# Performance work log

Hardware: AMD Instinct MI355X
Metric: run time of the kernel (lower is better)

Reference implementation:

```python
import jax, jax.numpy as jnp
import numpy as np

B, S, D, H = 2, 2048, 1024, 16
DK = D // H


def setup_inputs() -> dict:
    key = jax.random.key(0)
    ks = jax.random.split(key, 12)
    s = 1.0 / np.sqrt(D)
    return {
        "query": jax.random.normal(ks[0], (B, S, D), dtype=jnp.float32),
        "key": jax.random.normal(ks[1], (B, S, D), dtype=jnp.float32),
        "value": jax.random.normal(ks[2], (B, S, D), dtype=jnp.float32),
        "mask": jax.random.randint(ks[3], (B, 1, 1, S), 0, 2, dtype=jnp.int32),
        "wq": jax.random.normal(ks[4], (D, D), dtype=jnp.float32) * s,
        "bq": jnp.zeros((D,), dtype=jnp.float32),
        "wk": jax.random.normal(ks[5], (D, D), dtype=jnp.float32) * s,
        "bk": jnp.zeros((D,), dtype=jnp.float32),
        "wv": jax.random.normal(ks[6], (D, D), dtype=jnp.float32) * s,
        "bv": jnp.zeros((D,), dtype=jnp.float32),
        "wo": jax.random.normal(ks[7], (D, D), dtype=jnp.float32) * s,
        "bo": jnp.zeros((D,), dtype=jnp.float32),
    }


def reference(query, key, value, mask, wq, bq, wk, bk, wv, bv, wo, bo):
    b, s, d = query.shape
    # torch Linear: y = x @ W^T + b, then split heads -> [B, H, S, dk]
    def proj(x, w, bias):
        return (x @ w.T + bias).reshape(b, -1, H, DK).transpose(0, 2, 1, 3)

    q = proj(query, wq, bq)
    k = proj(key, wk, bk)
    v = proj(value, wv, bv)

    scores = jnp.einsum("bhqd,bhkd->bhqk", q, k) / jnp.sqrt(jnp.float32(DK))
    scores = jnp.where(mask == 0, jnp.float32(-1e9), scores)
    attn = jax.nn.softmax(scores, axis=-1)  # [B,H,S,S]
    x = jnp.einsum("bhqk,bhkd->bhqd", attn, v)
    x = x.transpose(0, 2, 1, 3).reshape(b, s, d)
    return x @ wo.T + bo
```

## Files before the change

kernel.cpp:

```cpp
#include <hip/hip_runtime.h>
#include <math.h>

#define B_  2
#define S_  2048
#define D_  1024
#define H_  16
#define DK_ 64

typedef unsigned short u16;
typedef unsigned int u32;
typedef __bf16 bf16x8 __attribute__((ext_vector_type(8)));
typedef float f32x4 __attribute__((ext_vector_type(4)));

typedef const __attribute__((address_space(1))) void* gas1_t;
typedef __attribute__((address_space(3))) void* las3_t;

__device__ __forceinline__ void gload_lds16(const void* g, void* l) {
    __builtin_amdgcn_global_load_lds((gas1_t)g, (las3_t)l, 16, 0, 0);
}

__device__ __forceinline__ u16 f2bf(float f) {
    union { float f; unsigned u; } v; v.f = f;
    return (u16)((v.u + 0x7fffu + ((v.u >> 16) & 1u)) >> 16);
}

__device__ __forceinline__ u32 pack_bf16_2(float lo, float hi) {
    union { float f; u32 u; } a, b;
    a.f = lo; b.f = hi;
    return __builtin_amdgcn_perm(b.u + 0x8000u, a.u + 0x8000u, 0x07060302u);
}

__global__ __launch_bounds__(256)
void cast_all(const float* __restrict__ q, const float* __restrict__ k,
              const float* __restrict__ v, const float* __restrict__ wq,
              const float* __restrict__ wk, const float* __restrict__ wv,
              const float* __restrict__ wo, const int* __restrict__ mask,
              u16* __restrict__ qb, u16* __restrict__ kb, u16* __restrict__ vb,
              u16* __restrict__ wqb, u16* __restrict__ wkb, u16* __restrict__ wvb,
              u16* __restrict__ wob, float* __restrict__ mfac,
              float* __restrict__ nmaskf)
{
    const int bi = blockIdx.x;
    const int tid = threadIdx.x;
    if (bi >= 16400) {
        const int b = bi - 16400;
        __shared__ int red[256];
        int c = 0;
#pragma unroll
        for (int j = 0; j < 8; ++j)
            c += (mask[b * S_ + tid * 8 + j] == 0) ? 1 : 0;
        red[tid] = c;
        __syncthreads();
        for (int s = 128; s > 0; s >>= 1) {
            if (tid < s) red[tid] += red[tid + s];
            __syncthreads();
        }
        if (tid == 0) nmaskf[b] = (float)red[0];
        return;
    }
    if (bi >= 16384) {
        const int idx = (bi - 16384) * 256 + tid;
        mfac[idx] = mask[idx] ? 1.0f : 0.0f;
        return;
    }
    const int i = bi * 256 + tid;
    const float* src; u16* dst; int off;
    if (i < 3 * 1048576) {
        const int seg = i >> 20; off = i & 1048575;
        src = (seg == 0) ? q : (seg == 1) ? k : v;
        dst = (seg == 0) ? qb : (seg == 1) ? kb : vb;
    } else {
        const int j = i - 3 * 1048576;
        const int seg = j >> 18; off = j & 262143;
        src = (seg == 0) ? wq : (seg == 1) ? wk : (seg == 2) ? wv : wo;
        dst = (seg == 0) ? wqb : (seg == 1) ? wkb : (seg == 2) ? wvb : wob;
    }
    const float4 val = ((const float4*)src)[off];
    uint2 o;
    o.x = pack_bf16_2(val.x, val.y);
    o.y = pack_bf16_2(val.z, val.w);
    ((uint2*)dst)[off] = o;
}

template<int BN>
__device__ __forceinline__ void gemm_body(
    const u16* __restrict__ A, const u16* __restrict__ W,
    const float* __restrict__ bias, void* __restrict__ outp,
    float scale, int mode, int m0, int n0,
    const float* __restrict__ rowfac, const float* __restrict__ colfac)
{
    constexpr int NJ = BN / 32;
    __shared__ u16 sA[128 * 64];
    __shared__ u16 sW[BN * 64];

    const int tid  = threadIdx.x;
    const int wave = tid >> 6, lane = tid & 63;
    const int quad = lane >> 4, l16 = lane & 15;
    const int wm = (wave >> 1) * 64;
    const int wn = (wave & 1) * (BN / 2);
    const int srow = lane >> 3;
    const int scol = ((lane & 7) ^ srow) * 8;
    const int sw7  = l16 & 7;

    f32x4 acc[4][NJ];
    const f32x4 zero = {0.f, 0.f, 0.f, 0.f};
#pragma unroll
    for (int i = 0; i < 4; ++i)
#pragma unroll
        for (int j = 0; j < NJ; ++j) acc[i][j] = zero;

    const u16* ast = A + (size_t)(m0 + wave * 8 + srow) * D_ + scol;
    const u16* wst = W + (size_t)(n0 + wave * 8 + srow) * D_ + scol;

    for (int k0 = 0; k0 < D_; k0 += 64) {
#pragma unroll
        for (int t = 0; t < 4; ++t)
            gload_lds16(ast + (size_t)t * 32 * D_ + k0, sA + (wave + t * 4) * 512);
        if (BN == 128) {
#pragma unroll
            for (int t = 0; t < 4; ++t)
                gload_lds16(wst + (size_t)t * 32 * D_ + k0, sW + (wave + t * 4) * 512);
        } else {
#pragma unroll
            for (int t = 0; t < 2; ++t)
                gload_lds16(wst + (size_t)t * 32 * D_ + k0, sW + (wave + t * 4) * 512);
        }
        __syncthreads();

#pragma unroll
        for (int kh = 0; kh < 2; ++kh) {
            const int phys = ((kh * 4 + quad) ^ sw7) * 8;
            bf16x8 af[4], bfr[NJ];
#pragma unroll
            for (int i = 0; i < 4; ++i)
                af[i] = *(const bf16x8*)(sA + (wm + i * 16 + l16) * 64 + phys);
#pragma unroll
            for (int j = 0; j < NJ; ++j)
                bfr[j] = *(const bf16x8*)(sW + (wn + j * 16 + l16) * 64 + phys);
#pragma unroll
            for (int i = 0; i < 4; ++i)
#pragma unroll
                for (int j = 0; j < NJ; ++j)
                    acc[i][j] = __builtin_amdgcn_mfma_f32_16x16x32_bf16(af[i], bfr[j], acc[i][j], 0, 0, 0);
        }
        __syncthreads();
    }

#pragma unroll
    for (int i = 0; i < 4; ++i) {
        float rf4[4];
        if (mode == 1 && rowfac) {
#pragma unroll
            for (int r = 0; r < 4; ++r)
                rf4[r] = rowfac[m0 + wm + i * 16 + quad * 4 + r];
        }
#pragma unroll
        for (int j = 0; j < NJ; ++j) {
            const int n = n0 + wn + j * 16 + l16;
            if (mode == 3) {
                const float cf = colfac ? colfac[n] : 1.0f;
#pragma unroll
                for (int r = 0; r < 4; ++r) {
                    const int mp = m0 + wm + i * 16 + quad * 4 + r;
                    ((u16*)outp)[(size_t)mp * (B_ * S_) + n] = f2bf((acc[i][j][r] + bias[mp]) * cf);
                }
            } else {
                const float bn = bias[n];
#pragma unroll
                for (int r = 0; r < 4; ++r) {
                    const int m = m0 + wm + i * 16 + quad * 4 + r;
                    float v = acc[i][j][r] + bn;
                    if (mode == 0) {
                        ((float*)outp)[(size_t)m * D_ + n] = v;
                    } else {
                        v *= scale;
                        if (rowfac) v *= rf4[r];
                        const int b = m >> 11, s = m & (S_ - 1);
                        const int h = n >> 6, dk = n & 63;
                        ((u16*)outp)[(((size_t)(b * H_ + h)) * S_ + s) * DK_ + dk] = f2bf(v);
                    }
                }
            }
        }
    }
}

__global__ __launch_bounds__(256)
void qkv_gemm(const u16* __restrict__ qin, const u16* __restrict__ kin, const u16* __restrict__ vin,
              const u16* __restrict__ wqb, const u16* __restrict__ wkb, const u16* __restrict__ wvb,
              const float* __restrict__ bq, const float* __restrict__ bk, const float* __restrict__ bv,
              u16* __restrict__ Qp, u16* __restrict__ Kp, u16* __restrict__ Vt,
              const float* __restrict__ mfac)
{
    const int z = blockIdx.z;
    if (z == 2) {
        gemm_body<128>(wvb, vin, bv, Vt, 1.0f, 3, blockIdx.x * 128, blockIdx.y * 128,
                       nullptr, mfac);
    } else {
        const u16* A = (z == 0) ? qin : kin;
        const u16* W = (z == 0) ? wqb : wkb;
        const float* bias = (z == 0) ? bq : bk;
        u16* outp = (z == 0) ? Qp : Kp;
        const float scale = (z == 0) ? 0.18033688011112042f : 1.0f;
        const float* rf = (z == 1) ? mfac : nullptr;
        gemm_body<128>(A, W, bias, outp, scale, 1, blockIdx.y * 128, blockIdx.x * 128,
                       rf, nullptr);
    }
}

__global__ __launch_bounds__(256)
void out_gemm(const u16* __restrict__ Xc, const u16* __restrict__ wob,
              const float* __restrict__ bo, float* __restrict__ out)
{
    gemm_body<64>(Xc, wob, bo, out, 1.0f, 0, blockIdx.y * 128, blockIdx.x * 64,
                  nullptr, nullptr);
}

__global__ __launch_bounds__(512, 4)
void attn_mfma(const u16* __restrict__ Qp, const u16* __restrict__ Kp,
               const u16* __restrict__ Vt, const float* __restrict__ nmaskf,
               u16* __restrict__ Xc)
{
    __shared__ u16 sPQ[8192];
    __shared__ u16 sKVraw[16384];

    const int tid  = threadIdx.x;
    const int wave = tid >> 6, lane = tid & 63;
    const int qg = wave & 3, kg = wave >> 2;
    const int quad = lane >> 4, l16 = lane & 15;
    const int qt = blockIdx.x & 15;
    const int bh = blockIdx.x >> 4;
    const int b  = bh >> 4;
    const int h  = bh & 15;
    const int lr  = lane >> 3;
    const int cl  = (lane & 7) ^ lr;
    const int sw7 = l16 & 7;

    const u16* Qb = Qp + ((size_t)bh * S_ + qt * 128) * DK_;
    const u16* Kb = Kp + (size_t)bh * S_ * DK_;
    const int vdk = (qg * 8 + lr) + 32 * (cl >> 2);
    const u16* Vsrc = Vt + (size_t)(h * 64 + vdk) * (B_ * S_) + b * S_ + (cl & 3) * 8;
    const u16* Ksrc = Kb + (size_t)(qg * 8 + lr) * DK_ + cl * 8;

#pragma unroll
    for (int t = 0; t < 2; ++t)
        gload_lds16(Qb + (size_t)(wave * 16 + t * 8 + lr) * DK_ + cl * 8,
                    sPQ + (wave * 2 + t) * 512);
    gload_lds16(Ksrc + (size_t)kg * 32 * DK_, sKVraw + (kg * 2) * 4096 + qg * 512);
    gload_lds16(Vsrc + kg * 32, sKVraw + (kg * 2) * 4096 + 2048 + qg * 512);
    __syncthreads();

    bf16x8 qf[2][2];
#pragma unroll
    for (int iq = 0; iq < 2; ++iq)
#pragma unroll
        for (int ks = 0; ks < 2; ++ks) {
            const int row = qg * 32 + iq * 16 + l16;
            const int c = (ks * 4 + quad) ^ sw7;
            qf[iq][ks] = *(const bf16x8*)(sPQ + row * 64 + c * 8);
        }
    u16* sPw = sPQ + wave * 1024;

    bf16x8 vones;
#pragma unroll
    for (int j = 0; j < 8; ++j) vones[j] = (__bf16)1.0f;

    f32x4 oacc[2][4];
    const f32x4 zero = {0.f, 0.f, 0.f, 0.f};
#pragma unroll
    for (int im = 0; im < 2; ++im)
#pragma unroll
        for (int nd = 0; nd < 4; ++nd) oacc[im][nd] = zero;
    f32x4 lfrag[2] = {zero, zero};

    const u16* kpre = Ksrc + (size_t)(kg + 2) * 32 * DK_;
    const u16* vpre = Vsrc + (kg + 2) * 32;

    for (int i = 0; i < 32; ++i) {
        __syncthreads();
        const int cur = i & 1;

        if (i < 31) {
            u16* dst = sKVraw + (kg * 2 + (cur ^ 1)) * 4096;
            gload_lds16(kpre, dst + qg * 512);
            gload_lds16(vpre, dst + 2048 + qg * 512);
            kpre += (size_t)2 * 32 * DK_;
            vpre += 64;
        }
        const u16* sK = sKVraw + (kg * 2 + cur) * 4096;
        const u16* sV = sK + 2048;

        f32x4 sfr[2][2];
#pragma unroll
        for (int in = 0; in < 2; ++in) {
            const int p0 = (quad ^ sw7) * 8;
            const int p1 = ((4 + quad) ^ sw7) * 8;
            const bf16x8 kf0 = *(const bf16x8*)(sK + (in * 16 + l16) * 64 + p0);
            const bf16x8 kf1 = *(const bf16x8*)(sK + (in * 16 + l16) * 64 + p1);
#pragma unroll
            for (int iq = 0; iq < 2; ++iq) {
                f32x4 t = __builtin_amdgcn_mfma_f32_16x16x32_bf16(kf0, qf[iq][0], zero, 0, 0, 0);
                sfr[iq][in] = __builtin_amdgcn_mfma_f32_16x16x32_bf16(kf1, qf[iq][1], t, 0, 0, 0);
            }
        }

#pragma unroll
        for (int iq = 0; iq < 2; ++iq)
#pragma unroll
            for (int in = 0; in < 2; ++in) {
                const float p0 = __builtin_amdgcn_exp2f(sfr[iq][in][0]);
                const float p1 = __builtin_amdgcn_exp2f(sfr[iq][in][1]);
                const float p2 = __builtin_amdgcn_exp2f(sfr[iq][in][2]);
                const float p3 = __builtin_amdgcn_exp2f(sfr[iq][in][3]);
                uint2 o;
                o.x = pack_bf16_2(p0, p1);
                o.y = pack_bf16_2(p2, p3);
                const int c = ((in * 2 + (quad >> 1)) + 4 * iq) ^ sw7;
                *(uint2*)(sPw + l16 * 64 + c * 8 + (quad & 1) * 4) = o;
            }

        bf16x8 pf[2];
#pragma unroll
        for (int im = 0; im < 2; ++im) {
            const int c = (quad + 4 * im) ^ sw7;
            pf[im] = *(const bf16x8*)(sPw + l16 * 64 + c * 8);
            lfrag[im] = __builtin_amdgcn_mfma_f32_16x16x32_bf16(pf[im], vones, lfrag[im], 0, 0, 0);
        }
#pragma unroll
        for (int nd = 0; nd < 4; ++nd) {
            const int prow = (nd & 1) * 16 + l16;
            const int vc = (quad + 4 * (nd >> 1)) ^ sw7;
            const bf16x8 vf = *(const bf16x8*)(sV + prow * 64 + vc * 8);
#pragma unroll
            for (int im = 0; im < 2; ++im)
                oacc[im][nd] = __builtin_amdgcn_mfma_f32_16x16x32_bf16(pf[im], vf, oacc[im][nd], 0, 0, 0);
        }
    }

    __syncthreads();
    float* sO = (float*)sKVraw;
    float* sL = (float*)sPQ;
    if (kg == 1) {
#pragma unroll
        for (int im = 0; im < 2; ++im) {
#pragma unroll
            for (int nd = 0; nd < 4; ++nd) {
                const int col = nd * 16 + l16;
                const int c = (im * 4 + quad) ^ sw7;
                *(f32x4*)((char*)(sO + qg * 2048) + col * 128 + c * 16) = oacc[im][nd];
            }
            if (l16 == 0) {
#pragma unroll
                for (int r = 0; r < 4; ++r)
                    sL[qg * 32 + im * 16 + quad * 4 + r] = lfrag[im][r];
            }
        }
    }
    __syncthreads();
    if (kg == 0) {
        const float nm = nmaskf[b];
#pragma unroll
        for (int im = 0; im < 2; ++im) {
            float linv[4];
#pragma unroll
            for (int r = 0; r < 4; ++r)
                linv[r] = __builtin_amdgcn_rcpf(
                    lfrag[im][r] + sL[qg * 32 + im * 16 + quad * 4 + r] - nm);
#pragma unroll
            for (int nd = 0; nd < 4; ++nd) {
                const int col = nd * 16 + l16;
                const int c = (im * 4 + quad) ^ sw7;
                const f32x4 o2 = *(const f32x4*)((const char*)(sO + qg * 2048) + col * 128 + c * 16);
#pragma unroll
                for (int r = 0; r < 4; ++r) {
                    const int s = qt * 128 + qg * 32 + im * 16 + quad * 4 + r;
                    Xc[((size_t)(b * S_ + s)) * D_ + h * 64 + col] =
                        f2bf((oacc[im][nd][r] + o2[r]) * linv[r]);
                }
            }
        }
    }
}

extern "C" void kernel_launch(void* const* d_in, const int* in_sizes, int n_in,
                              void* d_out, int out_size, void* d_ws, size_t ws_size,
                              hipStream_t stream)
{
    (void)in_sizes; (void)n_in; (void)out_size; (void)ws_size;

    const float* query = (const float*)d_in[0];
    const float* key   = (const float*)d_in[1];
    const float* value = (const float*)d_in[2];
    const int*   mask  = (const int*)d_in[3];
    const float* wq    = (const float*)d_in[4];
    const float* bq    = (const float*)d_in[5];
    const float* wk    = (const float*)d_in[6];
    const float* bk    = (const float*)d_in[7];
    const float* wv    = (const float*)d_in[8];
    const float* bv    = (const float*)d_in[9];
    const float* wo    = (const float*)d_in[10];
    const float* bo    = (const float*)d_in[11];

    const size_t NE = (size_t)B_ * S_ * D_;
    const size_t WE = (size_t)D_ * D_;

    u16* qb  = (u16*)d_ws;
    u16* kb  = qb + NE;
    u16* vb  = kb + NE;
    u16* wqb = vb + NE;
    u16* wkb = wqb + WE;
    u16* wvb = wkb + WE;
    u16* wob = wvb + WE;
    u16* Qp  = wob + WE;
    u16* Kp  = Qp + NE;
    u16* Vt  = Kp + NE;
    float* mfac   = (float*)(Vt + NE);
    float* nmaskf = mfac + 4096;
    u16* Xc  = qb;

    cast_all<<<16402, 256, 0, stream>>>(query, key, value, wq, wk, wv, wo, mask,
                                        qb, kb, vb, wqb, wkb, wvb, wob, mfac, nmaskf);

    qkv_gemm<<<dim3(D_ / 128, (B_ * S_) / 128, 3), 256, 0, stream>>>(
        qb, kb, vb, wqb, wkb, wvb, bq, bk, bv, Qp, Kp, Vt, mfac);

    attn_mfma<<<dim3(B_ * H_ * (S_ / 128)), 512, 0, stream>>>(Qp, Kp, Vt, nmaskf, Xc);

    out_gemm<<<dim3(D_ / 64, (B_ * S_) / 128), 256, 0, stream>>>(Xc, wob, bo, (float*)d_out);
}
```

Baseline: 226.9 us.

## Switch attention to 32x32x16 MFMA with register-shuffled P operand

Rewrites the attention inner loop to use 32x32x16 bf16 MFMA instead of 16x16x32, computing S^T tiles so the exponentiated probabilities can be rearranged into the PV A-operand through cross-half lane shuffles rather than a round trip through LDS. The row sum is now computed with VALU adds plus a shuffle instead of an MFMA against a ones vector. It also adds s_setprio around the MFMA groups and reworks the epilogue layout to match. The aim is to cut LDS traffic and the extra MFMAs per iteration, at the cost of more VALU and permute work and more accumulator registers.

```diff
diff --git a/kernel.cpp b/kernel.cpp
--- a/kernel.cpp
+++ b/kernel.cpp
@@ -11,6 +11,8 @@
 typedef unsigned int u32;
 typedef __bf16 bf16x8 __attribute__((ext_vector_type(8)));
 typedef float f32x4 __attribute__((ext_vector_type(4)));
+typedef float f32x16 __attribute__((ext_vector_type(16)));
+typedef u32 u32x4 __attribute__((ext_vector_type(4)));
 
 typedef const __attribute__((address_space(1))) void* gas1_t;
 typedef __attribute__((address_space(3))) void* las3_t;
@@ -221,20 +223,20 @@
                const u16* __restrict__ Vt, const float* __restrict__ nmaskf,
                u16* __restrict__ Xc)
 {
-    __shared__ u16 sPQ[8192];
+    __shared__ u16 sQ[128 * 64];
     __shared__ u16 sKVraw[16384];
 
     const int tid  = threadIdx.x;
     const int wave = tid >> 6, lane = tid & 63;
     const int qg = wave & 3, kg = wave >> 2;
-    const int quad = lane >> 4, l16 = lane & 15;
+    const int l31 = lane & 31, hi = lane >> 5;
     const int qt = blockIdx.x & 15;
     const int bh = blockIdx.x >> 4;
     const int b  = bh >> 4;
     const int h  = bh & 15;
     const int lr  = lane >> 3;
     const int cl  = (lane & 7) ^ lr;
-    const int sw7 = l16 & 7;
+    const int sw5 = l31 & 7;
 
     const u16* Qb = Qp + ((size_t)bh * S_ + qt * 128) * DK_;
     const u16* Kb = Kp + (size_t)bh * S_ * DK_;
@@ -245,33 +247,24 @@
 #pragma unroll
     for (int t = 0; t < 2; ++t)
         gload_lds16(Qb + (size_t)(wave * 16 + t * 8 + lr) * DK_ + cl * 8,
-                    sPQ + (wave * 2 + t) * 512);
+                    sQ + (wave * 2 + t) * 512);
     gload_lds16(Ksrc + (size_t)kg * 32 * DK_, sKVraw + (kg * 2) * 4096 + qg * 512);
     gload_lds16(Vsrc + kg * 32, sKVraw + (kg * 2) * 4096 + 2048 + qg * 512);
     __syncthreads();
 
-    bf16x8 qf[2][2];
-#pragma unroll
-    for (int iq = 0; iq < 2; ++iq)
-#pragma unroll
-        for (int ks = 0; ks < 2; ++ks) {
-            const int row = qg * 32 + iq * 16 + l16;
-            const int c = (ks * 4 + quad) ^ sw7;
-            qf[iq][ks] = *(const bf16x8*)(sPQ + row * 64 + c * 8);
-        }
-    u16* sPw = sPQ + wave * 1024;
-
-    bf16x8 vones;
-#pragma unroll
-    for (int j = 0; j < 8; ++j) vones[j] = (__bf16)1.0f;
-
-    f32x4 oacc[2][4];
-    const f32x4 zero = {0.f, 0.f, 0.f, 0.f};
-#pragma unroll
-    for (int im = 0; im < 2; ++im)
-#pragma unroll
-        for (int nd = 0; nd < 4; ++nd) oacc[im][nd] = zero;
-    f32x4 lfrag[2] = {zero, zero};
+    bf16x8 qf[4];
+#pragma unroll
+    for (int ks = 0; ks < 4; ++ks) {
+        const int row = qg * 32 + l31;
+        const int phys = (ks * 2 + hi) ^ sw5;
+        qf[ks] = *(const bf16x8*)(sQ + row * 64 + phys * 8);
+    }
+
+    f32x16 oc[2];
+    const f32x16 z16 = {0.f,0.f,0.f,0.f,0.f,0.f,0.f,0.f,
+                        0.f,0.f,0.f,0.f,0.f,0.f,0.f,0.f};
+    oc[0] = z16; oc[1] = z16;
+    float lsum = 0.f;
 
     const u16* kpre = Ksrc + (size_t)(kg + 2) * 32 * DK_;
     const u16* vpre = Vsrc + (kg + 2) * 32;
@@ -290,93 +283,101 @@
         const u16* sK = sKVraw + (kg * 2 + cur) * 4096;
         const u16* sV = sK + 2048;
 
-        f32x4 sfr[2][2];
-#pragma unroll
-        for (int in = 0; in < 2; ++in) {
-            const int p0 = (quad ^ sw7) * 8;
-            const int p1 = ((4 + quad) ^ sw7) * 8;
-            const bf16x8 kf0 = *(const bf16x8*)(sK + (in * 16 + l16) * 64 + p0);
-            const bf16x8 kf1 = *(const bf16x8*)(sK + (in * 16 + l16) * 64 + p1);
-#pragma unroll
-            for (int iq = 0; iq < 2; ++iq) {
-                f32x4 t = __builtin_amdgcn_mfma_f32_16x16x32_bf16(kf0, qf[iq][0], zero, 0, 0, 0);
-                sfr[iq][in] = __builtin_amdgcn_mfma_f32_16x16x32_bf16(kf1, qf[iq][1], t, 0, 0, 0);
+        f32x16 sfr;
+        {
+            const bf16x8 k0 = *(const bf16x8*)(sK + l31 * 64 + (((0 * 2 + hi) ^ sw5)) * 8);
+            const bf16x8 k1 = *(const bf16x8*)(sK + l31 * 64 + (((1 * 2 + hi) ^ sw5)) * 8);
+            const bf16x8 k2 = *(const bf16x8*)(sK + l31 * 64 + (((2 * 2 + hi) ^ sw5)) * 8);
+            const bf16x8 k3 = *(const bf16x8*)(sK + l31 * 64 + (((3 * 2 + hi) ^ sw5)) * 8);
+            __builtin_amdgcn_s_setprio(1);
+            sfr = __builtin_amdgcn_mfma_f32_32x32x16_bf16(k0, qf[0], z16, 0, 0, 0);
+            sfr = __builtin_amdgcn_mfma_f32_32x32x16_bf16(k1, qf[1], sfr, 0, 0, 0);
+            sfr = __builtin_amdgcn_mfma_f32_32x32x16_bf16(k2, qf[2], sfr, 0, 0, 0);
+            sfr = __builtin_amdgcn_mfma_f32_32x32x16_bf16(k3, qf[3], sfr, 0, 0, 0);
+            __builtin_amdgcn_s_setprio(0);
+        }
+
+        float p[16];
+#pragma unroll
+        for (int r = 0; r < 16; ++r) p[r] = __builtin_amdgcn_exp2f(sfr[r]);
+
+        {
+            const float s0 = (p[0] + p[1]) + (p[2] + p[3]);
+            const float s1 = (p[4] + p[5]) + (p[6] + p[7]);
+            const float s2 = (p[8] + p[9]) + (p[10] + p[11]);
+            const float s3 = (p[12] + p[13]) + (p[14] + p[15]);
+            float rsum = (s0 + s1) + (s2 + s3);
+            rsum += __shfl_xor(rsum, 32);
+            lsum += rsum;
+        }
+
+        const u32 W00 = pack_bf16_2(p[0], p[1]);
+        const u32 W01 = pack_bf16_2(p[2], p[3]);
+        const u32 W10 = pack_bf16_2(p[4], p[5]);
+        const u32 W11 = pack_bf16_2(p[6], p[7]);
+        const u32 W20 = pack_bf16_2(p[8], p[9]);
+        const u32 W21 = pack_bf16_2(p[10], p[11]);
+        const u32 W30 = pack_bf16_2(p[12], p[13]);
+        const u32 W31 = pack_bf16_2(p[14], p[15]);
+
+        const bool hib = (hi != 0);
+        const u32 X0 = hib ? W00 : W10;
+        const u32 X1 = hib ? W01 : W11;
+        const u32 X2 = hib ? W20 : W30;
+        const u32 X3 = hib ? W21 : W31;
+        const u32 Y0 = (u32)__shfl_xor((int)X0, 32);
+        const u32 Y1 = (u32)__shfl_xor((int)X1, 32);
+        const u32 Y2 = (u32)__shfl_xor((int)X2, 32);
+        const u32 Y3 = (u32)__shfl_xor((int)X3, 32);
+        u32x4 A0 = { hib ? Y0 : W00, hib ? Y1 : W01, hib ? W10 : Y0, hib ? W11 : Y1 };
+        u32x4 A1 = { hib ? Y2 : W20, hib ? Y3 : W21, hib ? W30 : Y2, hib ? W31 : Y3 };
+        const bf16x8 pa0 = *(const bf16x8*)&A0;
+        const bf16x8 pa1 = *(const bf16x8*)&A1;
+
+        {
+            const bf16x8 v00 = *(const bf16x8*)(sV + l31 * 64 + (((0 + 0 + hi) ^ sw5)) * 8);
+            const bf16x8 v01 = *(const bf16x8*)(sV + l31 * 64 + (((0 + 2 + hi) ^ sw5)) * 8);
+            const bf16x8 v10 = *(const bf16x8*)(sV + l31 * 64 + (((4 + 0 + hi) ^ sw5)) * 8);
+            const bf16x8 v11 = *(const bf16x8*)(sV + l31 * 64 + (((4 + 2 + hi) ^ sw5)) * 8);
+            __builtin_amdgcn_s_setprio(1);
+            oc[0] = __builtin_amdgcn_mfma_f32_32x32x16_bf16(pa0, v00, oc[0], 0, 0, 0);
+            oc[0] = __builtin_amdgcn_mfma_f32_32x32x16_bf16(pa1, v01, oc[0], 0, 0, 0);
+            oc[1] = __builtin_amdgcn_mfma_f32_32x32x16_bf16(pa0, v10, oc[1], 0, 0, 0);
+            oc[1] = __builtin_amdgcn_mfma_f32_32x32x16_bf16(pa1, v11, oc[1], 0, 0, 0);
+            __builtin_amdgcn_s_setprio(0);
+        }
+    }
+
+    __syncthreads();
+    float* sL = (float*)sQ;
+    float* sO = (float*)sKVraw;
+    if (hi == 0) sL[kg * 128 + qg * 32 + l31] = lsum;
+    if (kg == 1) {
+#pragma unroll
+        for (int dh = 0; dh < 2; ++dh)
+#pragma unroll
+            for (int g = 0; g < 4; ++g) {
+                f32x4 t = { oc[dh][g * 4 + 0], oc[dh][g * 4 + 1],
+                            oc[dh][g * 4 + 2], oc[dh][g * 4 + 3] };
+                *(f32x4*)(sO + qg * 2048 + ((dh * 4 + g) * 2 + hi) * 128 + l31 * 4) = t;
             }
-        }
-
-#pragma unroll
-        for (int iq = 0; iq < 2; ++iq)
-#pragma unroll
-            for (int in = 0; in < 2; ++in) {
-                const float p0 = __builtin_amdgcn_exp2f(sfr[iq][in][0]);
-                const float p1 = __builtin_amdgcn_exp2f(sfr[iq][in][1]);
-                const float p2 = __builtin_amdgcn_exp2f(sfr[iq][in][2]);
-                const float p3 = __builtin_amdgcn_exp2f(sfr[iq][in][3]);
-                uint2 o;
-                o.x = pack_bf16_2(p0, p1);
-                o.y = pack_bf16_2(p2, p3);
-                const int c = ((in * 2 + (quad >> 1)) + 4 * iq) ^ sw7;
-                *(uint2*)(sPw + l16 * 64 + c * 8 + (quad & 1) * 4) = o;
-            }
-
-        bf16x8 pf[2];
-#pragma unroll
-        for (int im = 0; im < 2; ++im) {
-            const int c = (quad + 4 * im) ^ sw7;
-            pf[im] = *(const bf16x8*)(sPw + l16 * 64 + c * 8);
-            lfrag[im] = __builtin_amdgcn_mfma_f32_16x16x32_bf16(pf[im], vones, lfrag[im], 0, 0, 0);
-        }
-#pragma unroll
-        for (int nd = 0; nd < 4; ++nd) {
-            const int prow = (nd & 1) * 16 + l16;
-            const int vc = (quad + 4 * (nd >> 1)) ^ sw7;
-            const bf16x8 vf = *(const bf16x8*)(sV + prow * 64 + vc * 8);
-#pragma unroll
-            for (int im = 0; im < 2; ++im)
-                oacc[im][nd] = __builtin_amdgcn_mfma_f32_16x16x32_bf16(pf[im], vf, oacc[im][nd], 0, 0, 0);
-        }
-    }
-
-    __syncthreads();
-    float* sO = (float*)sKVraw;
-    float* sL = (float*)sPQ;
-    if (kg == 1) {
-#pragma unroll
-        for (int im = 0; im < 2; ++im) {
-#pragma unroll
-            for (int nd = 0; nd < 4; ++nd) {
-                const int col = nd * 16 + l16;
-                const int c = (im * 4 + quad) ^ sw7;
-                *(f32x4*)((char*)(sO + qg * 2048) + col * 128 + c * 16) = oacc[im][nd];
-            }
-            if (l16 == 0) {
-#pragma unroll
-                for (int r = 0; r < 4; ++r)
-                    sL[qg * 32 + im * 16 + quad * 4 + r] = lfrag[im][r];
-            }
-        }
     }
     __syncthreads();
     if (kg == 0) {
         const float nm = nmaskf[b];
 #pragma unroll
-        for (int im = 0; im < 2; ++im) {
-            float linv[4];
-#pragma unroll
-            for (int r = 0; r < 4; ++r)
-                linv[r] = __builtin_amdgcn_rcpf(
-                    lfrag[im][r] + sL[qg * 32 + im * 16 + quad * 4 + r] - nm);
-#pragma unroll
-            for (int nd = 0; nd < 4; ++nd) {
-                const int col = nd * 16 + l16;
-                const int c = (im * 4 + quad) ^ sw7;
-                const f32x4 o2 = *(const f32x4*)((const char*)(sO + qg * 2048) + col * 128 + c * 16);
-#pragma unroll
-                for (int r = 0; r < 4; ++r) {
-                    const int s = qt * 128 + qg * 32 + im * 16 + quad * 4 + r;
-                    Xc[((size_t)(b * S_ + s)) * D_ + h * 64 + col] =
-                        f2bf((oacc[im][nd][r] + o2[r]) * linv[r]);
-                }
+        for (int g = 0; g < 4; ++g) {
+            const f32x4 oA = *(const f32x4*)(sO + qg * 2048 + ((0 + g) * 2 + hi) * 128 + l31 * 4);
+            const f32x4 oB = *(const f32x4*)(sO + qg * 2048 + ((4 + g) * 2 + hi) * 128 + l31 * 4);
+#pragma unroll
+            for (int rr = 0; rr < 4; ++rr) {
+                const int qrow = rr + 8 * g + 4 * hi;
+                const float inv = __builtin_amdgcn_rcpf(
+                    sL[qg * 32 + qrow] + sL[128 + qg * 32 + qrow] - nm);
+                const int s = qt * 128 + qg * 32 + qrow;
+                const size_t base = ((size_t)(b * S_ + s)) * D_ + h * 64 + l31;
+                Xc[base]      = f2bf((oc[0][g * 4 + rr] + oA[rr]) * inv);
+                Xc[base + 32] = f2bf((oc[1][g * 4 + rr] + oB[rr]) * inv);
             }
         }
     }
```

Result: no change. 227.1 us (+0.1%).
